# Kernel tuning notes

Measured on AMD Instinct MI355X. Metric: run time of the kernel, lower is better.

The kernel has to match this reference:

```python
import jax, jax.numpy as jnp
import numpy as np

DIM = 512        # model dim
MOE_DIM = 256    # expert hidden dim
E = 64           # n_routed experts
G = 8            # n_routed_group
TOPK_G = 4       # n_topk_group
K = 8            # n_experts_per_tok
SCALE = 2.5      # routed_scale
CAP = 1024


def setup_inputs() -> dict:
    key = jax.random.key(0)
    ks = jax.random.split(key, 6)
    x = jax.random.normal(ks[0], (4, 512, DIM), jnp.float32)
    gate_w = jax.random.normal(ks[1], (E, DIM), jnp.float32) / np.sqrt(DIM).astype(np.float32)
    gate_b = jax.random.normal(ks[2], (E,), jnp.float32) * 0.01
    w1 = jax.random.normal(ks[3], (E, DIM, MOE_DIM), jnp.float32) / np.sqrt(DIM).astype(np.float32)
    w3 = jax.random.normal(ks[4], (E, DIM, MOE_DIM), jnp.float32) / np.sqrt(DIM).astype(np.float32)
    w2 = jax.random.normal(ks[5], (E, MOE_DIM, DIM), jnp.float32) / np.sqrt(MOE_DIM).astype(np.float32)
    return {"x": x, "gate_w": gate_w, "gate_b": gate_b, "w1": w1, "w3": w3, "w2": w2}


def _gate(x2, gate_w, gate_b):
    # x2: [T, DIM] -> (weights [T,K], indices [T,K])
    T = x2.shape[0]
    scores = jax.nn.sigmoid(x2 @ gate_w.T)                      # [T, E]
    s = (scores + gate_b).reshape(T, G, E // G)                  # grouped scores
    group_scores = jax.lax.top_k(s, 2)[0].sum(-1)                # [T, G] sum of top-2 per group
    top_groups = jax.lax.top_k(group_scores, TOPK_G)[1]          # [T, TOPK_G]
    gmask = jnp.zeros((T, G), bool).at[jnp.arange(T)[:, None], top_groups].set(True)
    s = jnp.where(gmask[..., None], s, -jnp.inf).reshape(T, E)
    idx = jax.lax.top_k(s, K)[1]                                 # [T, K]
    w = jnp.take_along_axis(scores, idx, axis=1)                 # original (pre-bias) scores
    w = w / w.sum(-1, keepdims=True) * SCALE
    return w, idx


def _moe_forward(x, gate_w, gate_b, w1, w3, w2):
    shape = x.shape
    x2 = x.reshape(-1, DIM)                                      # [T, DIM]
    T = x2.shape[0]
    w, idx = _gate(x2, gate_w, gate_b)
    flat_e = idx.reshape(-1)                                     # [T*K]
    # position of each (token, slot) within its expert's buffer, in order
    oh = (flat_e[:, None] == jnp.arange(E)[None, :]).astype(jnp.int32)  # [T*K, E]
    pos = (jnp.cumsum(oh, axis=0) * oh).sum(-1) - 1              # [T*K]
    x_rep = jnp.repeat(x2, K, axis=0)                            # [T*K, DIM]
    # dispatch into per-expert buffers [E, CAP, DIM]
    xb = jnp.zeros((E, CAP, DIM), x2.dtype).at[flat_e, pos].set(x_rep, mode='drop')
    h = jax.nn.silu(jnp.einsum('ecd,edm->ecm', xb, w1)) * jnp.einsum('ecd,edm->ecm', xb, w3)
    yb = jnp.einsum('ecm,emd->ecd', h, w2)                       # [E, CAP, DIM]
    # combine: gather back and weight
    y = yb.at[flat_e, pos].get(mode='fill', fill_value=0.0) * w.reshape(-1)[:, None]
    return y.reshape(T, K, DIM).sum(1).reshape(shape)


def reference(x, gate_w, gate_b, w1, w3, w2):
    return _moe_forward(x, gate_w, gate_b, w1, w3, w2)
```

## Files before the change

### kernel.cpp

```cpp
#include <hip/hip_runtime.h>

#define T_TOK 2048
#define DIM   512
#define MOE   256
#define NE    64
#define NG    8
#define TOPKG 4
#define TOPK  8
#define CAP   1024
#define MOE_SCALE 2.5f

typedef float f32x4 __attribute__((ext_vector_type(4)));
typedef short s16x8 __attribute__((ext_vector_type(8)));

__device__ __forceinline__ unsigned short f2bf(float f) {
    unsigned u = __builtin_bit_cast(unsigned, f);
    unsigned r = (u + 0x7fffu + ((u >> 16) & 1u)) >> 16;
    return (unsigned short)r;
}
__device__ __forceinline__ unsigned pk2(float lo, float hi) {
    return (unsigned)f2bf(lo) | ((unsigned)f2bf(hi) << 16);
}

__global__ __launch_bounds__(256) void gwt_k(const float* __restrict__ gw,
                                             float* __restrict__ gwT)
{
    int idx = blockIdx.x * 256 + threadIdx.x;
    int e = idx >> 9, k = idx & 511;
    gwT[(size_t)(k >> 2) * 256 + e * 4 + (k & 3)] = gw[idx];
}

__global__ __launch_bounds__(256) void gate_fused_k(const float* __restrict__ x,
                                                    const float* __restrict__ gwT,
                                                    const float* __restrict__ gb,
                                                    int* __restrict__ counts,
                                                    int* __restrict__ etok,
                                                    float* __restrict__ wt_of,
                                                    short* __restrict__ xb)
{
    __shared__ float xs[4][512];
    int w = threadIdx.x >> 6, lane = threadIdx.x & 63;
    int t = blockIdx.x * 4 + w;

    {
        const float4* xr = (const float4*)(x + (size_t)t * DIM);
        float4 v0 = xr[lane * 2], v1 = xr[lane * 2 + 1];
        *(float4*)&xs[w][lane * 8]     = v0;
        *(float4*)&xs[w][lane * 8 + 4] = v1;
        short o[8];
        o[0] = (short)f2bf(v0.x); o[1] = (short)f2bf(v0.y);
        o[2] = (short)f2bf(v0.z); o[3] = (short)f2bf(v0.w);
        o[4] = (short)f2bf(v1.x); o[5] = (short)f2bf(v1.y);
        o[6] = (short)f2bf(v1.z); o[7] = (short)f2bf(v1.w);
        *(s16x8*)(xb + (size_t)t * DIM + lane * 8) = *(const s16x8*)o;
    }
    __syncthreads();

    const float4* gt = (const float4*)gwT;
    float a0 = 0.f, a1 = 0.f, a2 = 0.f, a3 = 0.f;
#pragma unroll 4
    for (int k4 = 0; k4 < 128; k4 += 4) {
        float4 g0 = gt[(k4 + 0) * 64 + lane];
        float4 g1 = gt[(k4 + 1) * 64 + lane];
        float4 g2 = gt[(k4 + 2) * 64 + lane];
        float4 g3 = gt[(k4 + 3) * 64 + lane];
        float4 x0 = *(const float4*)&xs[w][(k4 + 0) * 4];
        float4 x1 = *(const float4*)&xs[w][(k4 + 1) * 4];
        float4 x2 = *(const float4*)&xs[w][(k4 + 2) * 4];
        float4 x3 = *(const float4*)&xs[w][(k4 + 3) * 4];
        a0 += g0.x * x0.x + g0.y * x0.y + g0.z * x0.z + g0.w * x0.w;
        a1 += g1.x * x1.x + g1.y * x1.y + g1.z * x1.z + g1.w * x1.w;
        a2 += g2.x * x2.x + g2.y * x2.y + g2.z * x2.z + g2.w * x2.w;
        a3 += g3.x * x3.x + g3.y * x3.y + g3.z * x3.z + g3.w * x3.w;
    }
    float acc = (a0 + a1) + (a2 + a3);
    float sc = 1.f / (1.f + __expf(-acc));
    float s  = sc + gb[lane];

    float m1 = s, m2 = -1e30f;
#pragma unroll
    for (int d = 1; d < 8; d <<= 1) {
        float o1 = __shfl_xor(m1, d);
        float o2 = __shfl_xor(m2, d);
        float n1 = fmaxf(m1, o1);
        float n2 = fmaxf(fminf(m1, o1), fmaxf(m2, o2));
        m1 = n1; m2 = n2;
    }
    float gv = m1 + m2;

    bool gkeep = false;
#pragma unroll
    for (int it = 0; it < TOPKG; ++it) {
        float m = gv;
#pragma unroll
        for (int d = 1; d < 64; d <<= 1) m = fmaxf(m, __shfl_xor(m, d));
        unsigned long long mask = __ballot(gv == m);
        int ldr = __ffsll(mask) - 1;
        if ((lane >> 3) == (ldr >> 3)) { gkeep = true; gv = -2e30f; }
    }
    float sv = gkeep ? s : -1e30f;

    float wsum = 0.f;
    int my_e = 0; float my_w = 0.f;
#pragma unroll
    for (int k = 0; k < TOPK; ++k) {
        float m = sv;
#pragma unroll
        for (int d = 1; d < 64; d <<= 1) m = fmaxf(m, __shfl_xor(m, d));
        unsigned long long mask = __ballot(sv == m);
        int l = __ffsll(mask) - 1;
        float wk = __shfl(sc, l);
        wsum += wk;
        if (lane == k) { my_e = l; my_w = wk; }
        if (lane == l) sv = -2e30f;
    }
    float scale = MOE_SCALE / wsum;
    if (lane < TOPK) {
        int p = atomicAdd(&counts[my_e], 1);
        int rid = t * TOPK + lane;
        bool ok = (p < CAP);
        if (ok) etok[my_e * CAP + p] = rid;
        wt_of[rid] = ok ? my_w * scale : 0.f;
    }
}

__global__ __launch_bounds__(64) void scan_k(const int* __restrict__ counts,
                                             int* __restrict__ tbase)
{
    int lane = threadIdx.x;
    int ne = min(counts[lane], CAP);
    int nt = (ne + 31) >> 5;
    int v = nt;
#pragma unroll
    for (int d = 1; d < 64; d <<= 1) {
        int o = __shfl_up(v, d);
        if (lane >= d) v += o;
    }
    tbase[lane] = v - nt;
}

__global__ __launch_bounds__(256, 4) void gemm1_k(const short* __restrict__ xb,
                                                  const float* __restrict__ w1,
                                                  const float* __restrict__ w3,
                                                  const int* __restrict__ counts,
                                                  const int* __restrict__ etok,
                                                  const int* __restrict__ tbase,
                                                  short* __restrict__ hgf)
{
    __shared__ short Bl[2][16][64][8];
    __shared__ short Ct[4][2][16][24];

    int e  = blockIdx.x & 63, cg = blockIdx.x >> 6;
    int n0 = cg * 16;
    int tid = threadIdx.x;
    int w = tid >> 6, lane = tid & 63;
    int q = lane >> 4, m16 = lane & 15;

    const float* W1e = w1 + (size_t)e * DIM * MOE + n0;
    const float* W3e = w3 + (size_t)e * DIM * MOE + n0;
#pragma unroll 4
    for (int it = 0; it < 8; ++it) {
        int idx = it * 256 + tid;
        int mat = idx >> 10;
        int rem = idx & 1023;
        int r2  = rem >> 2;
        int cq  = (rem & 3) * 4;
        int k   = r2 * 2;
        int kt = k >> 5, qf = (k >> 3) & 3, j0 = k & 7;
        const float* p = (mat ? W3e : W1e) + (size_t)k * MOE + cq;
        float4 lo = *(const float4*)p;
        float4 hi = *(const float4*)(p + MOE);
        unsigned* b = (unsigned*)&Bl[mat][kt][qf * 16 + cq][j0];
        b[0]  = pk2(lo.x, hi.x);
        b[4]  = pk2(lo.y, hi.y);
        b[8]  = pk2(lo.z, hi.z);
        b[12] = pk2(lo.w, hi.w);
    }
    __syncthreads();

    int ne = min(counts[e], CAP);
    int nt = (ne + 31) >> 5;
    int G0 = tbase[e];
    const int* el = etok + e * CAP;

    for (int T = w; T < nt; T += 4) {
        int row0 = T * 32 + m16, row1 = T * 32 + 16 + m16;
        int tok0 = el[row0 < ne ? row0 : ne - 1] >> 3;
        int tok1 = el[row1 < ne ? row1 : ne - 1] >> 3;
        const short* A0 = xb + (size_t)tok0 * DIM + q * 8;
        const short* A1 = xb + (size_t)tok1 * DIM + q * 8;

        f32x4 acc[2][2];
#pragma unroll
        for (int j = 0; j < 2; ++j)
#pragma unroll
            for (int m = 0; m < 2; ++m) acc[j][m] = (f32x4)0.f;

        s16x8 a0 = *(const s16x8*)(A0);
        s16x8 a1 = *(const s16x8*)(A1);
#pragma unroll
        for (int kt = 0; kt < 16; ++kt) {
            s16x8 a0n, a1n;
            if (kt < 15) {
                a0n = *(const s16x8*)(A0 + (kt + 1) * 32);
                a1n = *(const s16x8*)(A1 + (kt + 1) * 32);
            }
            s16x8 b1 = *(const s16x8*)&Bl[0][kt][lane][0];
            s16x8 b3 = *(const s16x8*)&Bl[1][kt][lane][0];
            acc[0][0] = __builtin_amdgcn_mfma_f32_16x16x32_bf16(a0, b1, acc[0][0], 0, 0, 0);
            acc[1][0] = __builtin_amdgcn_mfma_f32_16x16x32_bf16(a1, b1, acc[1][0], 0, 0, 0);
            acc[0][1] = __builtin_amdgcn_mfma_f32_16x16x32_bf16(a0, b3, acc[0][1], 0, 0, 0);
            acc[1][1] = __builtin_amdgcn_mfma_f32_16x16x32_bf16(a1, b3, acc[1][1], 0, 0, 0);
            a0 = a0n; a1 = a1n;
        }

#pragma unroll
        for (int sub = 0; sub < 2; ++sub)
#pragma unroll
            for (int r = 0; r < 4; ++r) {
                float g = acc[sub][0][r];
                float u = acc[sub][1][r];
                float hv = g / (1.f + __expf(-g)) * u;
                Ct[w][sub][q * 4 + r][m16] = (short)f2bf(hv);
            }
        int sub = q >> 1;
        s16x8 hv8 = *(const s16x8*)&Ct[w][sub][m16][(q & 1) * 8];
        size_t slot = ((size_t)(G0 + T) * 8 + (cg >> 1)) * 2 + sub;
        *(s16x8*)(hgf + slot * 512 + ((cg & 1) * 2 + (q & 1)) * 128 + m16 * 8) = hv8;
    }
}

__global__ __launch_bounds__(256, 4) void gemm2_k(const short* __restrict__ hgf,
                                                  const float* __restrict__ w2,
                                                  const int* __restrict__ counts,
                                                  const int* __restrict__ etok,
                                                  const int* __restrict__ tbase,
                                                  short* __restrict__ ybuf)
{
    __shared__ short Bl[2][8][64][8];

    int e  = blockIdx.x & 63, cg = blockIdx.x >> 6;
    int n0 = cg * 32;
    int tid = threadIdx.x;
    int w = tid >> 6, lane = tid & 63;
    int q = lane >> 4, m16 = lane & 15;

    const float* W2e = w2 + (size_t)e * MOE * DIM + n0;
#pragma unroll 4
    for (int it = 0; it < 4; ++it) {
        int idx = it * 256 + tid;
        int r2  = idx >> 3;
        int cq  = (idx & 7) * 4;
        int k   = r2 * 2;
        int kt2 = k >> 5, qf = (k >> 3) & 3, j0 = k & 7;
        int s = cq >> 4, c15 = cq & 15;
        const float* p = W2e + (size_t)k * DIM + cq;
        float4 lo = *(const float4*)p;
        float4 hi = *(const float4*)(p + DIM);
        unsigned* b = (unsigned*)&Bl[s][kt2][qf * 16 + c15][j0];
        b[0]  = pk2(lo.x, hi.x);
        b[4]  = pk2(lo.y, hi.y);
        b[8]  = pk2(lo.z, hi.z);
        b[12] = pk2(lo.w, hi.w);
    }
    __syncthreads();

    int ne = min(counts[e], CAP);
    int nt = (ne + 31) >> 5;
    int G0 = tbase[e];
    const int* el = etok + e * CAP;

    for (int T = w; T < nt; T += 4) {
        const short* A = hgf + (size_t)(G0 + T) * 8192 + lane * 8;

        f32x4 acc[2][2];
#pragma unroll
        for (int j = 0; j < 2; ++j)
#pragma unroll
            for (int m = 0; m < 2; ++m) acc[j][m] = (f32x4)0.f;

        s16x8 a0 = *(const s16x8*)(A);
        s16x8 a1 = *(const s16x8*)(A + 512);
#pragma unroll
        for (int kt = 0; kt < 8; ++kt) {
            s16x8 a0n, a1n;
            if (kt < 7) {
                a0n = *(const s16x8*)(A + (size_t)((kt + 1) * 2 + 0) * 512);
                a1n = *(const s16x8*)(A + (size_t)((kt + 1) * 2 + 1) * 512);
            }
            s16x8 b0 = *(const s16x8*)&Bl[0][kt][lane][0];
            s16x8 b1 = *(const s16x8*)&Bl[1][kt][lane][0];
            acc[0][0] = __builtin_amdgcn_mfma_f32_16x16x32_bf16(a0, b0, acc[0][0], 0, 0, 0);
            acc[1][0] = __builtin_amdgcn_mfma_f32_16x16x32_bf16(a1, b0, acc[1][0], 0, 0, 0);
            acc[0][1] = __builtin_amdgcn_mfma_f32_16x16x32_bf16(a0, b1, acc[0][1], 0, 0, 0);
            acc[1][1] = __builtin_amdgcn_mfma_f32_16x16x32_bf16(a1, b1, acc[1][1], 0, 0, 0);
            a0 = a0n; a1 = a1n;
        }

#pragma unroll
        for (int sub = 0; sub < 2; ++sub)
#pragma unroll
            for (int s = 0; s < 2; ++s)
#pragma unroll
                for (int r = 0; r < 4; ++r) {
                    int row = T * 32 + sub * 16 + q * 4 + r;
                    if (row < ne)
                        ybuf[(size_t)el[row] * DIM + n0 + s * 16 + m16] =
                            (short)f2bf(acc[sub][s][r]);
                }
    }
}

__global__ __launch_bounds__(256) void combine_k(const short* __restrict__ ybuf,
                                                 const float* __restrict__ wt_of,
                                                 float* __restrict__ out)
{
    int t = blockIdx.x;
    int tid = threadIdx.x;
    const int* yb = (const int*)ybuf;
    float sx = 0.f, sy = 0.f;
#pragma unroll
    for (int k = 0; k < TOPK; ++k) {
        float wk = wt_of[t * TOPK + k];
        int v = yb[(size_t)(t * TOPK + k) * (DIM / 2) + tid];
        float lo = __builtin_bit_cast(float, (unsigned)v << 16);
        float hi = __builtin_bit_cast(float, (unsigned)v & 0xffff0000u);
        sx += wk * lo;
        sy += wk * hi;
    }
    float2 o = {sx, sy};
    ((float2*)out)[(size_t)t * (DIM / 2) + tid] = o;
}

extern "C" void kernel_launch(void* const* d_in, const int* in_sizes, int n_in,
                              void* d_out, int out_size, void* d_ws, size_t ws_size,
                              hipStream_t stream)
{
    const float* x  = (const float*)d_in[0];
    const float* gw = (const float*)d_in[1];
    const float* gb = (const float*)d_in[2];
    const float* w1 = (const float*)d_in[3];
    const float* w3 = (const float*)d_in[4];
    const float* w2 = (const float*)d_in[5];

    char* ws = (char*)d_ws;
    short* xb    = (short*)(ws);
    short* hgf   = (short*)(ws + 2097152);
    short* ybuf  = (short*)(ws + 11534336);
    float* gwT   = (float*)(ws + 28311552);
    int*   etok  = (int*)  (ws + 28442624);
    float* wt_of = (float*)(ws + 28704768);
    int*   counts= (int*)  (ws + 28770304);
    int*   tbase = (int*)  (ws + 28770560);

    hipMemsetAsync(counts, 0, NE * 4, stream);

    gwt_k<<<128, 256, 0, stream>>>(gw, gwT);
    gate_fused_k<<<T_TOK / 4, 256, 0, stream>>>(x, gwT, gb, counts, etok, wt_of, xb);
    scan_k<<<1, 64, 0, stream>>>(counts, tbase);
    gemm1_k<<<NE * 16, 256, 0, stream>>>(xb, w1, w3, counts, etok, tbase, hgf);
    gemm2_k<<<NE * 16, 256, 0, stream>>>(hgf, w2, counts, etok, tbase, ybuf);
    combine_k<<<T_TOK, 256, 0, stream>>>(ybuf, wt_of, (float*)d_out);
}
```

Before: 265.3 us.

## Drop scan kernel, index hidden buffer by routing id, widen GEMM tiles

```diff
diff --git a/kernel.cpp b/kernel.cpp
--- a/kernel.cpp
+++ b/kernel.cpp
@@ -124,34 +124,17 @@
     }
 }
 
-__global__ __launch_bounds__(64) void scan_k(const int* __restrict__ counts,
-                                             int* __restrict__ tbase)
-{
-    int lane = threadIdx.x;
-    int ne = min(counts[lane], CAP);
-    int nt = (ne + 31) >> 5;
-    int v = nt;
-#pragma unroll
-    for (int d = 1; d < 64; d <<= 1) {
-        int o = __shfl_up(v, d);
-        if (lane >= d) v += o;
-    }
-    tbase[lane] = v - nt;
-}
-
-__global__ __launch_bounds__(256, 4) void gemm1_k(const short* __restrict__ xb,
+__global__ __launch_bounds__(512, 4) void gemm1_k(const short* __restrict__ xb,
                                                   const float* __restrict__ w1,
                                                   const float* __restrict__ w3,
                                                   const int* __restrict__ counts,
                                                   const int* __restrict__ etok,
-                                                  const int* __restrict__ tbase,
-                                                  short* __restrict__ hgf)
-{
-    __shared__ short Bl[2][16][64][8];
-    __shared__ short Ct[4][2][16][24];
+                                                  short* __restrict__ hbuf)
+{
+    __shared__ short Bl[2][2][16][64][8];
 
     int e  = blockIdx.x & 63, cg = blockIdx.x >> 6;
-    int n0 = cg * 16;
+    int n0 = cg * 32;
     int tid = threadIdx.x;
     int w = tid >> 6, lane = tid & 63;
     int q = lane >> 4, m16 = lane & 15;
@@ -160,17 +143,18 @@
     const float* W3e = w3 + (size_t)e * DIM * MOE + n0;
 #pragma unroll 4
     for (int it = 0; it < 8; ++it) {
-        int idx = it * 256 + tid;
-        int mat = idx >> 10;
-        int rem = idx & 1023;
-        int r2  = rem >> 2;
-        int cq  = (rem & 3) * 4;
+        int idx = it * 512 + tid;
+        int mat = idx >> 11;
+        int rem = idx & 2047;
+        int r2  = rem >> 3;
+        int cq  = (rem & 7) * 4;
         int k   = r2 * 2;
         int kt = k >> 5, qf = (k >> 3) & 3, j0 = k & 7;
+        int s = cq >> 4, c15 = cq & 15;
         const float* p = (mat ? W3e : W1e) + (size_t)k * MOE + cq;
         float4 lo = *(const float4*)p;
         float4 hi = *(const float4*)(p + MOE);
-        unsigned* b = (unsigned*)&Bl[mat][kt][qf * 16 + cq][j0];
+        unsigned* b = (unsigned*)&Bl[mat][s][kt][qf * 16 + c15][j0];
         b[0]  = pk2(lo.x, hi.x);
         b[4]  = pk2(lo.y, hi.y);
         b[8]  = pk2(lo.z, hi.z);
@@ -180,67 +164,65 @@
 
     int ne = min(counts[e], CAP);
     int nt = (ne + 31) >> 5;
-    int G0 = tbase[e];
     const int* el = etok + e * CAP;
 
-    for (int T = w; T < nt; T += 4) {
+    for (int T = w; T < nt; T += 8) {
         int row0 = T * 32 + m16, row1 = T * 32 + 16 + m16;
         int tok0 = el[row0 < ne ? row0 : ne - 1] >> 3;
         int tok1 = el[row1 < ne ? row1 : ne - 1] >> 3;
         const short* A0 = xb + (size_t)tok0 * DIM + q * 8;
         const short* A1 = xb + (size_t)tok1 * DIM + q * 8;
 
-        f32x4 acc[2][2];
-#pragma unroll
-        for (int j = 0; j < 2; ++j)
-#pragma unroll
-            for (int m = 0; m < 2; ++m) acc[j][m] = (f32x4)0.f;
-
-        s16x8 a0 = *(const s16x8*)(A0);
-        s16x8 a1 = *(const s16x8*)(A1);
+        f32x4 acc[2][2][2];
+#pragma unroll
+        for (int i = 0; i < 2; ++i)
+#pragma unroll
+            for (int j = 0; j < 2; ++j)
+#pragma unroll
+                for (int m = 0; m < 2; ++m) acc[i][j][m] = (f32x4)0.f;
+
 #pragma unroll
         for (int kt = 0; kt < 16; ++kt) {
-            s16x8 a0n, a1n;
-            if (kt < 15) {
-                a0n = *(const s16x8*)(A0 + (kt + 1) * 32);
-                a1n = *(const s16x8*)(A1 + (kt + 1) * 32);
+            s16x8 a0 = *(const s16x8*)(A0 + kt * 32);
+            s16x8 a1 = *(const s16x8*)(A1 + kt * 32);
+#pragma unroll
+            for (int s = 0; s < 2; ++s) {
+                s16x8 b1 = *(const s16x8*)&Bl[0][s][kt][lane][0];
+                s16x8 b3 = *(const s16x8*)&Bl[1][s][kt][lane][0];
+                acc[0][0][s] = __builtin_amdgcn_mfma_f32_16x16x32_bf16(a0, b1, acc[0][0][s], 0, 0, 0);
+                acc[1][0][s] = __builtin_amdgcn_mfma_f32_16x16x32_bf16(a1, b1, acc[1][0][s], 0, 0, 0);
+                acc[0][1][s] = __builtin_amdgcn_mfma_f32_16x16x32_bf16(a0, b3, acc[0][1][s], 0, 0, 0);
+                acc[1][1][s] = __builtin_amdgcn_mfma_f32_16x16x32_bf16(a1, b3, acc[1][1][s], 0, 0, 0);
             }
-            s16x8 b1 = *(const s16x8*)&Bl[0][kt][lane][0];
-            s16x8 b3 = *(const s16x8*)&Bl[1][kt][lane][0];
-            acc[0][0] = __builtin_amdgcn_mfma_f32_16x16x32_bf16(a0, b1, acc[0][0], 0, 0, 0);
-            acc[1][0] = __builtin_amdgcn_mfma_f32_16x16x32_bf16(a1, b1, acc[1][0], 0, 0, 0);
-            acc[0][1] = __builtin_amdgcn_mfma_f32_16x16x32_bf16(a0, b3, acc[0][1], 0, 0, 0);
-            acc[1][1] = __builtin_amdgcn_mfma_f32_16x16x32_bf16(a1, b3, acc[1][1], 0, 0, 0);
-            a0 = a0n; a1 = a1n;
         }
 
 #pragma unroll
         for (int sub = 0; sub < 2; ++sub)
 #pragma unroll
-            for (int r = 0; r < 4; ++r) {
-                float g = acc[sub][0][r];
-                float u = acc[sub][1][r];
-                float hv = g / (1.f + __expf(-g)) * u;
-                Ct[w][sub][q * 4 + r][m16] = (short)f2bf(hv);
-            }
-        int sub = q >> 1;
-        s16x8 hv8 = *(const s16x8*)&Ct[w][sub][m16][(q & 1) * 8];
-        size_t slot = ((size_t)(G0 + T) * 8 + (cg >> 1)) * 2 + sub;
-        *(s16x8*)(hgf + slot * 512 + ((cg & 1) * 2 + (q & 1)) * 128 + m16 * 8) = hv8;
-    }
-}
-
-__global__ __launch_bounds__(256, 4) void gemm2_k(const short* __restrict__ hgf,
+            for (int s = 0; s < 2; ++s)
+#pragma unroll
+                for (int r = 0; r < 4; ++r) {
+                    int row = T * 32 + sub * 16 + q * 4 + r;
+                    if (row < ne) {
+                        float g = acc[sub][0][s][r];
+                        float u = acc[sub][1][s][r];
+                        float hv = g / (1.f + __expf(-g)) * u;
+                        hbuf[(size_t)el[row] * MOE + n0 + s * 16 + m16] = (short)f2bf(hv);
+                    }
+                }
+    }
+}
+
+__global__ __launch_bounds__(512, 4) void gemm2_k(const short* __restrict__ hbuf,
                                                   const float* __restrict__ w2,
                                                   const int* __restrict__ counts,
                                                   const int* __restrict__ etok,
-                                                  const int* __restrict__ tbase,
                                                   short* __restrict__ ybuf)
 {
-    __shared__ short Bl[2][8][64][8];
+    __shared__ short Bl[4][8][64][8];
 
     int e  = blockIdx.x & 63, cg = blockIdx.x >> 6;
-    int n0 = cg * 32;
+    int n0 = cg * 64;
     int tid = threadIdx.x;
     int w = tid >> 6, lane = tid & 63;
     int q = lane >> 4, m16 = lane & 15;
@@ -248,16 +230,16 @@
     const float* W2e = w2 + (size_t)e * MOE * DIM + n0;
 #pragma unroll 4
     for (int it = 0; it < 4; ++it) {
-        int idx = it * 256 + tid;
-        int r2  = idx >> 3;
-        int cq  = (idx & 7) * 4;
+        int idx = it * 512 + tid;
+        int r2  = idx >> 4;
+        int cq  = (idx & 15) * 4;
         int k   = r2 * 2;
-        int kt2 = k >> 5, qf = (k >> 3) & 3, j0 = k & 7;
+        int kt = k >> 5, qf = (k >> 3) & 3, j0 = k & 7;
         int s = cq >> 4, c15 = cq & 15;
         const float* p = W2e + (size_t)k * DIM + cq;
         float4 lo = *(const float4*)p;
         float4 hi = *(const float4*)(p + DIM);
-        unsigned* b = (unsigned*)&Bl[s][kt2][qf * 16 + c15][j0];
+        unsigned* b = (unsigned*)&Bl[s][kt][qf * 16 + c15][j0];
         b[0]  = pk2(lo.x, hi.x);
         b[4]  = pk2(lo.y, hi.y);
         b[8]  = pk2(lo.z, hi.z);
@@ -267,40 +249,37 @@
 
     int ne = min(counts[e], CAP);
     int nt = (ne + 31) >> 5;
-    int G0 = tbase[e];
     const int* el = etok + e * CAP;
 
-    for (int T = w; T < nt; T += 4) {
-        const short* A = hgf + (size_t)(G0 + T) * 8192 + lane * 8;
-
-        f32x4 acc[2][2];
-#pragma unroll
-        for (int j = 0; j < 2; ++j)
-#pragma unroll
-            for (int m = 0; m < 2; ++m) acc[j][m] = (f32x4)0.f;
-
-        s16x8 a0 = *(const s16x8*)(A);
-        s16x8 a1 = *(const s16x8*)(A + 512);
+    for (int T = w; T < nt; T += 8) {
+        int row0 = T * 32 + m16, row1 = T * 32 + 16 + m16;
+        int rid0 = el[row0 < ne ? row0 : ne - 1];
+        int rid1 = el[row1 < ne ? row1 : ne - 1];
+        const short* A0 = hbuf + (size_t)rid0 * MOE + q * 8;
+        const short* A1 = hbuf + (size_t)rid1 * MOE + q * 8;
+
+        f32x4 acc[2][4];
+#pragma unroll
+        for (int i = 0; i < 2; ++i)
+#pragma unroll
+            for (int j = 0; j < 4; ++j) acc[i][j] = (f32x4)0.f;
+
 #pragma unroll
         for (int kt = 0; kt < 8; ++kt) {
-            s16x8 a0n, a1n;
-            if (kt < 7) {
-                a0n = *(const s16x8*)(A + (size_t)((kt + 1) * 2 + 0) * 512);
-                a1n = *(const s16x8*)(A + (size_t)((kt + 1) * 2 + 1) * 512);
+            s16x8 a0 = *(const s16x8*)(A0 + kt * 32);
+            s16x8 a1 = *(const s16x8*)(A1 + kt * 32);
+#pragma unroll
+            for (int s = 0; s < 4; ++s) {
+                s16x8 b = *(const s16x8*)&Bl[s][kt][lane][0];
+                acc[0][s] = __builtin_amdgcn_mfma_f32_16x16x32_bf16(a0, b, acc[0][s], 0, 0, 0);
+                acc[1][s] = __builtin_amdgcn_mfma_f32_16x16x32_bf16(a1, b, acc[1][s], 0, 0, 0);
             }
-            s16x8 b0 = *(const s16x8*)&Bl[0][kt][lane][0];
-            s16x8 b1 = *(const s16x8*)&Bl[1][kt][lane][0];
-            acc[0][0] = __builtin_amdgcn_mfma_f32_16x16x32_bf16(a0, b0, acc[0][0], 0, 0, 0);
-            acc[1][0] = __builtin_amdgcn_mfma_f32_16x16x32_bf16(a1, b0, acc[1][0], 0, 0, 0);
-            acc[0][1] = __builtin_amdgcn_mfma_f32_16x16x32_bf16(a0, b1, acc[0][1], 0, 0, 0);
-            acc[1][1] = __builtin_amdgcn_mfma_f32_16x16x32_bf16(a1, b1, acc[1][1], 0, 0, 0);
-            a0 = a0n; a1 = a1n;
         }
 
 #pragma unroll
         for (int sub = 0; sub < 2; ++sub)
 #pragma unroll
-            for (int s = 0; s < 2; ++s)
+            for (int s = 0; s < 4; ++s)
 #pragma unroll
                 for (int r = 0; r < 4; ++r) {
                     int row = T * 32 + sub * 16 + q * 4 + r;
@@ -345,20 +324,18 @@
 
     char* ws = (char*)d_ws;
     short* xb    = (short*)(ws);
-    short* hgf   = (short*)(ws + 2097152);
-    short* ybuf  = (short*)(ws + 11534336);
-    float* gwT   = (float*)(ws + 28311552);
-    int*   etok  = (int*)  (ws + 28442624);
-    float* wt_of = (float*)(ws + 28704768);
-    int*   counts= (int*)  (ws + 28770304);
-    int*   tbase = (int*)  (ws + 28770560);
+    short* hbuf  = (short*)(ws + 2097152);
+    short* ybuf  = (short*)(ws + 10485760);
+    float* gwT   = (float*)(ws + 27262976);
+    int*   etok  = (int*)  (ws + 27394048);
+    float* wt_of = (float*)(ws + 27656192);
+    int*   counts= (int*)  (ws + 27721728);
 
     hipMemsetAsync(counts, 0, NE * 4, stream);
 
     gwt_k<<<128, 256, 0, stream>>>(gw, gwT);
     gate_fused_k<<<T_TOK / 4, 256, 0, stream>>>(x, gwT, gb, counts, etok, wt_of, xb);
-    scan_k<<<1, 64, 0, stream>>>(counts, tbase);
-    gemm1_k<<<NE * 16, 256, 0, stream>>>(xb, w1, w3, counts, etok, tbase, hgf);
-    gemm2_k<<<NE * 16, 256, 0, stream>>>(hgf, w2, counts, etok, tbase, ybuf);
+    gemm1_k<<<NE * 8, 512, 0, stream>>>(xb, w1, w3, counts, etok, hbuf);
+    gemm2_k<<<NE * 8, 512, 0, stream>>>(hbuf, w2, counts, etok, ybuf);
     combine_k<<<T_TOK, 256, 0, stream>>>(ybuf, wt_of, (float*)d_out);
 }
```

Result: slower. 330.8 us (+24.7%).
